# Kernel tuning notes

Hardware: AMD Instinct MI355X
Metric: run time of the kernel (lower is better)

The kernel has to match this reference:

```python
import jax, jax.numpy as jnp
import numpy as np

DILATION = 64
KERNEL = 2

def setup_inputs() -> dict:
    key = jax.random.key(0)
    k1, k2 = jax.random.split(key)
    x = jax.random.normal(k1, (16, 64, 16384), dtype=jnp.float32)
    w = jax.random.normal(k2, (64, 64, KERNEL), dtype=jnp.float32) * 0.1
    return {"x": x, "w": w}

def _causal_dilated_conv(x, w):
    # left-pad by dilation*(kernel_size-1) for causality
    pad = DILATION * (KERNEL - 1)
    xp = jnp.pad(x, ((0, 0), (0, 0), (pad, 0)))
    return jax.lax.conv_general_dilated(
        xp, w,
        window_strides=(1,),
        padding='VALID',
        rhs_dilation=(DILATION,),
        dimension_numbers=('NCH', 'OIH', 'NCH'))

def reference(x, w):
    y = _causal_dilated_conv(x, w)          # [B, C_out, T]
    return jnp.tanh(y) * jax.nn.sigmoid(y)  # fused gate
```

## Files before the change

### kernel.cpp

```cpp
#include <hip/hip_runtime.h>


#define B_ 16
#define C_ 64
#define T_ 16384

typedef __attribute__((ext_vector_type(8))) short short8;
typedef __attribute__((ext_vector_type(4))) float f32x4;

union Frag { short8 s; unsigned u[4]; };

__device__ __forceinline__ unsigned bf16_rne(float f) {
    unsigned u = __float_as_uint(f);
    return (u + 0x7fffu + ((u >> 16) & 1u)) >> 16;
}

__device__ __forceinline__ unsigned pack_rne(float a, float b) {
    unsigned ua = __float_as_uint(a), ub = __float_as_uint(b);
    unsigned ra = ua + 0x7fffu + ((ua >> 16) & 1u);
    unsigned rb = ub + 0x7fffu + ((ub >> 16) & 1u);
    return (ra >> 16) | (rb & 0xffff0000u);
}

#define EPILOGUE(A, KK)                                                     \
    _Pragma("unroll")                                                       \
    for (int s = 0; s < 4; ++s) {                                           \
        float4 o4;                                                          \
        _Pragma("unroll")                                                   \
        for (int r = 0; r < 4; ++r) {                                       \
            float y = fmaxf((A)[s][r], -30.f);                              \
            float u = __expf(-y);                                           \
            ((float*)&o4)[r] = (1.f - u) *                                  \
                __builtin_amdgcn_rcpf(__builtin_fmaf(u, u, 1.f));           \
        }                                                                   \
        *(float4*)(ob + (KK) * 64 + 16 * s + 4 * q) = o4;                   \
    }

#define STAGE_WRITE(F, BANK)                                                \
    _Pragma("unroll")                                                       \
    for (int e = 0; e < 4; ++e) {                                           \
        const int rr = 4 * tq + e;                                          \
        const int so = (BANK) * 4096 + rr * 64 +                            \
                       (((c4 >> 1) ^ (rr & 7)) * 8) + ((c4 & 1) * 4);       \
        unsigned u0 = pack_rne(((const float*)&(F)[0])[e],                  \
                               ((const float*)&(F)[1])[e]);                 \
        unsigned u1 = pack_rne(((const float*)&(F)[2])[e],                  \
                               ((const float*)&(F)[3])[e]);                 \
        *(uint2*)(&xs[so]) = make_uint2(u0, u1);                            \
    }

__global__ __launch_bounds__(256, 4) void conv_gate_wide(
    const float* __restrict__ x,
    const float* __restrict__ w,
    float* __restrict__ out)
{
    __shared__ unsigned short xs[3 * 64 * 64];

    const int tid = threadIdx.x;
    const int bid = blockIdx.x;
    const int wg  = (bid & 7) * 128 + (bid >> 3);
    const int b   = wg >> 6;
    const int seg = wg & 63;
    const int t0  = seg << 8;
    const float* xb = x + (size_t)b * C_ * T_;

    const int c4 = tid >> 4;
    const int tq = tid & 15;
    const float* xgb = xb + (size_t)(4 * c4) * T_ + 4 * tq;

    float4 fa[4], fb[4];
    if (seg > 0) {
        #pragma unroll
        for (int i = 0; i < 4; ++i)
            fa[i] = *(const float4*)(xgb + (size_t)i * T_ + (t0 - 64));
    } else {
        #pragma unroll
        for (int i = 0; i < 4; ++i) fa[i] = make_float4(0.f, 0.f, 0.f, 0.f);
    }
    #pragma unroll
    for (int i = 0; i < 4; ++i)
        fb[i] = *(const float4*)(xgb + (size_t)i * T_ + t0);

    const int lane = tid & 63;
    const int wid  = tid >> 6;
    const int m    = lane & 15;
    const int q    = lane >> 4;
    const int co   = wid * 16 + m;

    Frag wh[2][2], wl[2][2];
    #pragma unroll
    for (int h = 0; h < 2; ++h) {
        const float* wp = w + co * 128 + h * 64 + q * 16;
        float f[16];
        #pragma unroll
        for (int v4 = 0; v4 < 4; ++v4) {
            float4 t4 = *(const float4*)(wp + 4 * v4);
            f[4*v4+0] = t4.x; f[4*v4+1] = t4.y; f[4*v4+2] = t4.z; f[4*v4+3] = t4.w;
        }
        #pragma unroll
        for (int p = 0; p < 2; ++p) {
            #pragma unroll
            for (int d = 0; d < 4; ++d) {
                float e0 = f[2*(2*d)   + p];
                float e1 = f[2*(2*d+1) + p];
                unsigned h0 = bf16_rne(e0), h1 = bf16_rne(e1);
                float r0 = e0 - __uint_as_float(h0 << 16);
                float r1 = e1 - __uint_as_float(h1 << 16);
                wh[p][h].u[d] = h0 | (h1 << 16);
                wl[p][h].u[d] = bf16_rne(r0) | (bf16_rne(r1) << 16);
            }
        }
    }

    STAGE_WRITE(fa, 0)
    STAGE_WRITE(fb, 1)

    const int n   = m;
    const int swb = n & 7;
    float* ob = out + ((size_t)b * C_ + wid * 16 + m) * T_ + t0;

    f32x4 acc2[2][4];

    __syncthreads();

    #pragma unroll
    for (int k = 0; k < 4; ++k) {
        float4 fv[4];
        if (k <= 2) {
            #pragma unroll
            for (int i = 0; i < 4; ++i)
                fv[i] = *(const float4*)(xgb + (size_t)i * T_ + (t0 + 64 * (k + 1)));
        }

        if (k >= 1) { EPILOGUE(acc2[(k & 1) ^ 1], k - 1); }

        f32x4* acc = acc2[k & 1];
        #pragma unroll
        for (int s = 0; s < 4; ++s) acc[s] = (f32x4){0.f, 0.f, 0.f, 0.f};
        #pragma unroll
        for (int u = 0; u < 8; ++u) {
            const int wnd   = k + (u >> 2);
            const int rbase = (wnd % 3) * 4096 + (16 * (u & 3) + n) * 64;
            Frag f0, f1;
            f0.s = *(const short8*)(&xs[rbase + ((q ^ swb) * 8)]);
            f1.s = *(const short8*)(&xs[rbase + (((4 + q) ^ swb) * 8)]);
            if (u < 4) {
                acc[u] = __builtin_amdgcn_mfma_f32_16x16x32_bf16(f0.s, wh[0][0].s, acc[u], 0, 0, 0);
                acc[u] = __builtin_amdgcn_mfma_f32_16x16x32_bf16(f0.s, wl[0][0].s, acc[u], 0, 0, 0);
                acc[u] = __builtin_amdgcn_mfma_f32_16x16x32_bf16(f1.s, wh[0][1].s, acc[u], 0, 0, 0);
                acc[u] = __builtin_amdgcn_mfma_f32_16x16x32_bf16(f1.s, wl[0][1].s, acc[u], 0, 0, 0);
            } else {
                const int s2 = u - 4;
                acc[s2] = __builtin_amdgcn_mfma_f32_16x16x32_bf16(f0.s, wh[1][0].s, acc[s2], 0, 0, 0);
                acc[s2] = __builtin_amdgcn_mfma_f32_16x16x32_bf16(f0.s, wl[1][0].s, acc[s2], 0, 0, 0);
                acc[s2] = __builtin_amdgcn_mfma_f32_16x16x32_bf16(f1.s, wh[1][1].s, acc[s2], 0, 0, 0);
                acc[s2] = __builtin_amdgcn_mfma_f32_16x16x32_bf16(f1.s, wl[1][1].s, acc[s2], 0, 0, 0);
            }
        }

        if (k <= 2) { STAGE_WRITE(fv, (k + 2) % 3) }

        if (k < 3) __syncthreads();
    }

    EPILOGUE(acc2[1], 3);
}

extern "C" void kernel_launch(void* const* d_in, const int* in_sizes, int n_in,
                              void* d_out, int out_size, void* d_ws, size_t ws_size,
                              hipStream_t stream) {
    const float* x = (const float*)d_in[0];
    const float* w = (const float*)d_in[1];
    float* out = (float*)d_out;
    conv_gate_wide<<<dim3(1024), dim3(256), 0, stream>>>(x, w, out);
}
```

Baseline: 123.8 us.

## Prefetch input windows earlier, add XOR swizzle, use LDS-only barrier

Issues the global loads for the next two input windows before the main loop and the fourth window right after the first stage write, which deepens the prefetch. The aim is to hide global load latency behind the MFMA work. It replaces __syncthreads with a barrier that waits only on LDS counters, so outstanding global loads no longer stall at each barrier. It also extends the LDS XOR swizzle with the upper row bits to reduce bank conflicts. In exchange, register pressure rises from holding two extra float4x4 buffers, which may hurt occupancy at 4 waves/EU.

```diff
diff --git a/kernel.cpp b/kernel.cpp
--- a/kernel.cpp
+++ b/kernel.cpp
@@ -22,6 +22,12 @@
     return (ra >> 16) | (rb & 0xffff0000u);
 }
 
+#define LBAR()                                                              \
+    do {                                                                    \
+        asm volatile("s_waitcnt lgkmcnt(0)" ::: "memory");                  \
+        __builtin_amdgcn_s_barrier();                                       \
+    } while (0)
+
 #define EPILOGUE(A, KK)                                                     \
     _Pragma("unroll")                                                       \
     for (int s = 0; s < 4; ++s) {                                           \
@@ -40,8 +46,9 @@
     _Pragma("unroll")                                                       \
     for (int e = 0; e < 4; ++e) {                                           \
         const int rr = 4 * tq + e;                                          \
+        const int sw = (rr & 7) ^ ((rr >> 3) & 7);                          \
         const int so = (BANK) * 4096 + rr * 64 +                            \
-                       (((c4 >> 1) ^ (rr & 7)) * 8) + ((c4 & 1) * 4);       \
+                       (((c4 >> 1) ^ sw) * 8) + ((c4 & 1) * 4);             \
         unsigned u0 = pack_rne(((const float*)&(F)[0])[e],                  \
                                ((const float*)&(F)[1])[e]);                 \
         unsigned u1 = pack_rne(((const float*)&(F)[2])[e],                  \
@@ -49,7 +56,7 @@
         *(uint2*)(&xs[so]) = make_uint2(u0, u1);                            \
     }
 
-__global__ __launch_bounds__(256, 4) void conv_gate_wide(
+__global__ __launch_bounds__(256, 4) void conv_gate_cnt(
     const float* __restrict__ x,
     const float* __restrict__ w,
     float* __restrict__ out)
@@ -68,7 +75,7 @@
     const int tq = tid & 15;
     const float* xgb = xb + (size_t)(4 * c4) * T_ + 4 * tq;
 
-    float4 fa[4], fb[4];
+    float4 fa[4], fb[4], fv[2][4];
     if (seg > 0) {
         #pragma unroll
         for (int i = 0; i < 4; ++i)
@@ -80,6 +87,12 @@
     #pragma unroll
     for (int i = 0; i < 4; ++i)
         fb[i] = *(const float4*)(xgb + (size_t)i * T_ + t0);
+    #pragma unroll
+    for (int i = 0; i < 4; ++i)
+        fv[0][i] = *(const float4*)(xgb + (size_t)i * T_ + (t0 + 64));
+    #pragma unroll
+    for (int i = 0; i < 4; ++i)
+        fv[1][i] = *(const float4*)(xgb + (size_t)i * T_ + (t0 + 128));
 
     const int lane = tid & 63;
     const int wid  = tid >> 6;
@@ -115,23 +128,14 @@
     STAGE_WRITE(fa, 0)
     STAGE_WRITE(fb, 1)
 
-    const int n   = m;
-    const int swb = n & 7;
     float* ob = out + ((size_t)b * C_ + wid * 16 + m) * T_ + t0;
 
     f32x4 acc2[2][4];
 
-    __syncthreads();
+    LBAR();
 
     #pragma unroll
     for (int k = 0; k < 4; ++k) {
-        float4 fv[4];
-        if (k <= 2) {
-            #pragma unroll
-            for (int i = 0; i < 4; ++i)
-                fv[i] = *(const float4*)(xgb + (size_t)i * T_ + (t0 + 64 * (k + 1)));
-        }
-
         if (k >= 1) { EPILOGUE(acc2[(k & 1) ^ 1], k - 1); }
 
         f32x4* acc = acc2[k & 1];
@@ -139,11 +143,13 @@
         for (int s = 0; s < 4; ++s) acc[s] = (f32x4){0.f, 0.f, 0.f, 0.f};
         #pragma unroll
         for (int u = 0; u < 8; ++u) {
-            const int wnd   = k + (u >> 2);
-            const int rbase = (wnd % 3) * 4096 + (16 * (u & 3) + n) * 64;
+            const int wnd  = k + (u >> 2);
+            const int rr_r = 16 * (u & 3) + m;
+            const int sw_r = (rr_r & 7) ^ ((rr_r >> 3) & 7);
+            const int rbase = (wnd % 3) * 4096 + rr_r * 64;
             Frag f0, f1;
-            f0.s = *(const short8*)(&xs[rbase + ((q ^ swb) * 8)]);
-            f1.s = *(const short8*)(&xs[rbase + (((4 + q) ^ swb) * 8)]);
+            f0.s = *(const short8*)(&xs[rbase + ((q ^ sw_r) * 8)]);
+            f1.s = *(const short8*)(&xs[rbase + (((4 + q) ^ sw_r) * 8)]);
             if (u < 4) {
                 acc[u] = __builtin_amdgcn_mfma_f32_16x16x32_bf16(f0.s, wh[0][0].s, acc[u], 0, 0, 0);
                 acc[u] = __builtin_amdgcn_mfma_f32_16x16x32_bf16(f0.s, wl[0][0].s, acc[u], 0, 0, 0);
@@ -158,9 +164,15 @@
             }
         }
 
-        if (k <= 2) { STAGE_WRITE(fv, (k + 2) % 3) }
+        if (k <= 2) { STAGE_WRITE(fv[k & 1], (k + 2) % 3) }
 
-        if (k < 3) __syncthreads();
+        if (k == 0) {
+            #pragma unroll
+            for (int i = 0; i < 4; ++i)
+                fv[0][i] = *(const float4*)(xgb + (size_t)i * T_ + (t0 + 192));
+        }
+
+        if (k < 3) LBAR();
     }
 
     EPILOGUE(acc2[1], 3);
@@ -172,5 +184,5 @@
     const float* x = (const float*)d_in[0];
     const float* w = (const float*)d_in[1];
     float* out = (float*)d_out;
-    conv_gate_wide<<<dim3(1024), dim3(256), 0, stream>>>(x, w, out);
+    conv_gate_cnt<<<dim3(1024), dim3(256), 0, stream>>>(x, w, out);
 }
```

New measurement: 120.4 us. 2.7% less time.
